# Kernel tuning notes

Hardware: AMD Instinct MI355X
Metric: run time of the kernel (lower is better)

Reference implementation:

```python
import jax, jax.numpy as jnp
import numpy as np

S, B, C, H, M = 384, 8, 1024, 16, 1536
CC = C // H


def setup_inputs() -> dict:
    key = jax.random.key(0)
    ks = jax.random.split(key, 8)
    x = jax.random.normal(ks[0], (S, B, C), dtype=jnp.float32)
    pe = jax.random.normal(ks[1], (S, B, C), dtype=jnp.float32)
    memory_k = jax.random.normal(ks[2], (M, B, H, CC), dtype=jnp.float32)
    memory_v = jax.random.normal(ks[3], (M, B, H, CC), dtype=jnp.float32)
    w_qkv = jax.random.normal(ks[4], (C, 3 * C), dtype=jnp.float32) * 0.02
    b_qkv = jnp.zeros((3 * C,), dtype=jnp.float32)
    w_out = jax.random.normal(ks[5], (C, C), dtype=jnp.float32) * 0.02
    b_out = jnp.zeros((C,), dtype=jnp.float32)
    terminal = jnp.zeros((B,), dtype=bool)
    # causal mask over the new tokens: True = masked (future positions)
    content_mask = jnp.broadcast_to(
        (jnp.arange(S)[None, :] > jnp.arange(S)[:, None])[:, :, None], (S, S, B))
    padding_mask = jnp.zeros((S, B), dtype=bool)  # True = padded
    memory_length = jax.random.randint(ks[6], (B,), 0, M, dtype=jnp.int32)
    return dict(x=x, positional_encoding=pe, memory_k=memory_k, memory_v=memory_v,
                w_qkv=w_qkv, b_qkv=b_qkv, w_out=w_out, b_out=b_out,
                terminal=terminal, content_mask=content_mask,
                padding_mask=padding_mask, memory_length=memory_length)


def reference(x, positional_encoding, memory_k, memory_v, w_qkv, b_qkv,
              w_out, b_out, terminal, content_mask, padding_mask, memory_length):
    s, b, c = x.shape
    # qkv projection
    qkv = (x + positional_encoding) @ w_qkv + b_qkv          # [s,b,3c]
    q, k, v = jnp.split(qkv, 3, axis=-1)
    q = q.reshape(s, b, H, CC)
    k = k.reshape(s, b, H, CC)
    v = v.reshape(s, b, H, CC)
    # clear_memory(terminal): zero lengths for terminal episodes
    mem_len = jnp.where(terminal, 0, memory_length)          # [b]
    # ragged memory concat expressed with fixed capacity M + padding mask
    k_full = jnp.concatenate([memory_k, k], axis=0)          # [M+s,b,H,CC]
    v_full = jnp.concatenate([memory_v, v], axis=0)
    mem_pad = jnp.arange(M)[:, None] >= mem_len[None, :]     # [M,b] True=masked
    kv_pad = jnp.concatenate([mem_pad, padding_mask], axis=0)  # [M+s,b]
    mem_content = jnp.zeros((s, M, b), dtype=bool)           # memory visible to all queries
    full_content = jnp.concatenate([mem_content, content_mask], axis=1)  # [s,M+s,b]
    mask = full_content | kv_pad[None, :, :]                 # [s,M+s,b]
    # attention
    scores = jnp.einsum('sbhc,tbhc->stbh', q, k_full) * (1.0 / np.sqrt(CC))
    scores = jnp.where(mask[:, :, :, None], jnp.float32(-1e9), scores)
    p = jax.nn.softmax(scores, axis=1)                       # [s,M+s,b,h]
    out = jnp.einsum('stbh,tbhc->sbhc', p, v_full).reshape(s, b, c)
    return out @ w_out + b_out
```

## Files before the change

### kernel.cpp

```cpp
#include <hip/hip_runtime.h>
#include <math.h>

#define S_DIM 384
#define B_DIM 8
#define C_DIM 1024
#define H_DIM 16
#define M_DIM 1536
#define CC_DIM 64
#define ROWS  (S_DIM * B_DIM)
#define N3C   (3 * C_DIM)
#define CHUNK 6
#define MAXS  5

typedef unsigned short u16;
typedef short bf8v  __attribute__((ext_vector_type(8)));
typedef short bf4v  __attribute__((ext_vector_type(4)));
typedef u16   us8   __attribute__((ext_vector_type(8)));
typedef u16   us4   __attribute__((ext_vector_type(4)));
typedef float f4v   __attribute__((ext_vector_type(4)));

__device__ __forceinline__ u16 f2bf(float f) {
    unsigned u = __float_as_uint(f);
    u += 0x7fffu + ((u >> 16) & 1u);
    return (u16)(u >> 16);
}
__device__ __forceinline__ float bf2f(u16 v) {
    return __uint_as_float(((unsigned)v) << 16);
}
#if __has_builtin(__builtin_amdgcn_exp2f)
#define EX2(x) __builtin_amdgcn_exp2f(x)
#else
#define EX2(x) __expf((x) * 0.69314718056f)
#endif
#define QSCALE (0.125f * 1.44269504f)

__device__ __forceinline__ unsigned cvtpk_bf16(float a, float b) {
    unsigned r;
    asm("v_cvt_pk_bf16_f32 %0, %1, %2" : "=v"(r) : "v"(a), "v"(b));
    return r;
}

__device__ __forceinline__ f4v mfma16x16x16bf16(bf4v a, bf4v b, f4v c) {
#if __has_builtin(__builtin_amdgcn_mfma_f32_16x16x16bf16_1k)
    return __builtin_amdgcn_mfma_f32_16x16x16bf16_1k(a, b, c, 0, 0, 0);
#else
    return c;
#endif
}

__device__ __forceinline__ void gload16(const u16* g, u16* l) {
    __builtin_amdgcn_global_load_lds(
        (const __attribute__((address_space(1))) void*)g,
        (__attribute__((address_space(3))) void*)l, 16, 0, 0);
}

__device__ __forceinline__ void tr_direct8(const float* __restrict__ in,
                                           u16* __restrict__ out,
                                           int R, int Cc, int r0, int c0, int tid) {
    const int c4 = c0 + (tid & 15) * 4;
    const int rq = r0 + (tid >> 4) * 8;
    float4 L[8];
    #pragma unroll
    for (int k = 0; k < 8; k++)
        L[k] = *(const float4*)(in + (size_t)(rq + k) * Cc + c4);
    #pragma unroll
    for (int j = 0; j < 4; j++) {
        us8 o;
        #pragma unroll
        for (int k = 0; k < 8; k++)
            o[k] = f2bf(((const float*)&L[k])[j]);
        *(us8*)(out + (size_t)(c4 + j) * R + rq) = o;
    }
}

__global__ __launch_bounds__(256) void prep_all(
    const float* __restrict__ x, const float* __restrict__ pe, u16* __restrict__ Abf,
    const float* __restrict__ wqkv, u16* __restrict__ Wqkvt,
    const float* __restrict__ wout, u16* __restrict__ Woutt,
    const float* __restrict__ mk, u16* __restrict__ mk_bf,
    const float* __restrict__ mv, u16* __restrict__ mv_t,
    const unsigned char* __restrict__ terminal, const int* __restrict__ mem_len)
{
    const int bid = blockIdx.x, tid = threadIdx.x;

    if (bid < 1536) {
        const int bh = bid & 127, tg = bid >> 7;
        const int t0 = tg * 128;
        const int b = bh >> 4;
        const int L = terminal[b] ? 0 : mem_len[b];
        const int Lc = ((L + 63) >> 6) << 6;
        if (t0 >= Lc) return;
        const int cc4 = (tid & 15) * 4;
        const int tq = t0 + (tid >> 4) * 8;
        float4 Lv[8];
        #pragma unroll
        for (int k = 0; k < 8; k++)
            Lv[k] = *(const float4*)(mv + ((size_t)(tq + k) * 128 + bh) * 64 + cc4);
        #pragma unroll
        for (int j = 0; j < 4; j++) {
            us8 o;
            #pragma unroll
            for (int k = 0; k < 8; k++)
                o[k] = f2bf(((const float*)&Lv[k])[j]);
            *(us8*)(mv_t + ((size_t)bh * 64 + cc4 + j) * M_DIM + tq) = o;
        }
    } else if (bid < 4608) {
        const int b6 = bid - 1536;
        const int b = b6 & 7, t0 = (b6 >> 3) * 4;
        const int L = terminal[b] ? 0 : mem_len[b];
        const int Lc = ((L + 63) >> 6) << 6;
        if (t0 >= Lc) return;
        const int r = t0 + (tid >> 6);
        const size_t rb = (size_t)r * 8192 + (size_t)b * 1024;
        const int cw = (tid & 63) * 4;
        float4 v[4];
        #pragma unroll
        for (int j = 0; j < 4; j++)
            v[j] = *(const float4*)(mk + rb + cw + j * 256);
        #pragma unroll
        for (int j = 0; j < 4; j++) {
            us4 o;
            o[0] = f2bf(v[j].x); o[1] = f2bf(v[j].y);
            o[2] = f2bf(v[j].z); o[3] = f2bf(v[j].w);
            *(us4*)(mk_bf + rb + cw + j * 256) = o;
        }
    } else if (bid < 5376) {
        size_t i0 = (size_t)(bid - 4608) * 4096 + tid * 16;
        float4 xv[4], pv[4];
        #pragma unroll
        for (int j = 0; j < 4; j++) {
            xv[j] = *(const float4*)(x + i0 + j * 4);
            pv[j] = *(const float4*)(pe + i0 + j * 4);
        }
        #pragma unroll
        for (int h8 = 0; h8 < 2; h8++) {
            us8 o;
            #pragma unroll
            for (int j = 0; j < 2; j++) {
                float4 a = xv[h8 * 2 + j], p = pv[h8 * 2 + j];
                o[j * 4 + 0] = f2bf(a.x + p.x);
                o[j * 4 + 1] = f2bf(a.y + p.y);
                o[j * 4 + 2] = f2bf(a.z + p.z);
                o[j * 4 + 3] = f2bf(a.w + p.w);
            }
            *(us8*)(Abf + i0 + h8 * 8) = o;
        }
    } else if (bid < 5760) {
        const int b2 = bid - 5376;
        tr_direct8(wqkv, Wqkvt, C_DIM, N3C, (b2 / 48) * 128, (b2 % 48) * 64, tid);
    } else {
        const int b3 = bid - 5760;
        tr_direct8(wout, Woutt, C_DIM, C_DIM, (b3 / 16) * 128, (b3 % 16) * 64, tid);
    }
}

__global__ __launch_bounds__(256) void qkv_gemm(
    const u16* __restrict__ Abf, const u16* __restrict__ Wt,
    const float* __restrict__ bias,
    u16* __restrict__ Qw, u16* __restrict__ Kw, u16* __restrict__ Vwt)
{
    __shared__ u16 smem[128 * 64 + 64 * 64];
    u16* As = smem;
    u16* Bs = smem + 128 * 64;
    u16* Cs = smem;

    const int tid = threadIdx.x;
    const int lane = tid & 63, w = tid >> 6;
    const int lr = lane & 15, quad = lane >> 4;
    const int wm = w >> 1, wn = w & 1;
    const int row0 = blockIdx.y * 128, col0 = blockIdx.x * 64;

    f4v acc[4][2];
    #pragma unroll
    for (int i = 0; i < 4; i++)
        #pragma unroll
        for (int j = 0; j < 2; j++)
            acc[i][j] = (f4v){0.f, 0.f, 0.f, 0.f};

    for (int k0 = 0; k0 < C_DIM; k0 += 64) {
        __syncthreads();
        #pragma unroll
        for (int j = 0; j < 4; j++) {
            int idx = j * 256 + tid;
            int r = idx >> 3, c = (idx & 7) ^ (r & 7);
            gload16(&Abf[(size_t)(row0 + r) * C_DIM + k0 + c * 8], &As[idx * 8]);
        }
        #pragma unroll
        for (int j = 0; j < 2; j++) {
            int idx = j * 256 + tid;
            int r = idx >> 3, c = (idx & 7) ^ (r & 7);
            gload16(&Wt[(size_t)(col0 + r) * C_DIM + k0 + c * 8], &Bs[idx * 8]);
        }
        __syncthreads();
        #pragma unroll
        for (int kh = 0; kh < 2; kh++) {
            bf8v a[4], b[2];
            #pragma unroll
            for (int mi = 0; mi < 4; mi++) {
                int row = wm * 64 + mi * 16 + lr;
                int p = (kh * 4 + quad) ^ (lr & 7);
                a[mi] = *(const bf8v*)&As[row * 64 + p * 8];
            }
            #pragma unroll
            for (int nj = 0; nj < 2; nj++) {
                int row = wn * 32 + nj * 16 + lr;
                int p = (kh * 4 + quad) ^ (lr & 7);
                b[nj] = *(const bf8v*)&Bs[row * 64 + p * 8];
            }
            #pragma unroll
            for (int mi = 0; mi < 4; mi++)
                #pragma unroll
                for (int nj = 0; nj < 2; nj++)
                    acc[mi][nj] = __builtin_amdgcn_mfma_f32_16x16x32_bf16(a[mi], b[nj], acc[mi][nj], 0, 0, 0);
        }
    }

    const int which = col0 >> 10;
    const int h = (col0 >> 6) & 15;
    const float qs = (which == 0) ? QSCALE : 1.0f;

    __syncthreads();
    #pragma unroll
    for (int nj = 0; nj < 2; nj++) {
        int col = col0 + wn * 32 + nj * 16 + lr;
        float bv = bias[col];
        #pragma unroll
        for (int mi = 0; mi < 4; mi++)
            #pragma unroll
            for (int reg = 0; reg < 4; reg++)
                Cs[(wm * 64 + mi * 16 + quad * 4 + reg) * 72 + wn * 32 + nj * 16 + lr] =
                    f2bf((acc[mi][nj][reg] + bv) * qs);
    }
    __syncthreads();

    if (which != 2) {
        u16* dstbuf = (which == 0) ? Qw : Kw;
        int r = tid >> 1, half = tid & 1;
        int rg = row0 + r, s = rg >> 3, bb = rg & 7;
        u16* drow = dstbuf + ((size_t)(bb * 16 + h) * S_DIM + s) * 64 + half * 32;
        #pragma unroll
        for (int i = 0; i < 4; i++)
            *(us8*)(drow + i * 8) = *(const us8*)&Cs[r * 72 + half * 32 + i * 8];
    } else {
        int cc = tid & 63, w4 = tid >> 6;
        int s0 = row0 >> 3;
        #pragma unroll
        for (int pb = 0; pb < 2; pb++) {
            int bb = w4 * 2 + pb;
            us8 v0, v1;
            #pragma unroll
            for (int sl = 0; sl < 8; sl++) {
                v0[sl] = Cs[(sl * 8 + bb) * 72 + cc];
                v1[sl] = Cs[((sl + 8) * 8 + bb) * 72 + cc];
            }
            u16* dr = Vwt + ((size_t)(bb * 16 + h) * 64 + cc) * S_DIM + s0;
            *(us8*)dr = v0;
            *(us8*)(dr + 8) = v1;
        }
    }
}

__global__ __launch_bounds__(256) void attn_split(
    const u16* __restrict__ Qw, const u16* __restrict__ Kw,
    const u16* __restrict__ mk_bf, const u16* __restrict__ Vwt,
    const u16* __restrict__ mv_t, const unsigned char* __restrict__ terminal,
    const int* __restrict__ mem_len, u16* __restrict__ Op, float* __restrict__ ml)
{
    __shared__ u16 KsAll[4][64 * 64];
    __shared__ u16 VsAll[4][64 * 64];

    const int tid = threadIdx.x;
    const int lane = tid & 63, w = tid >> 6;
    const int lr = lane & 15, quad = lane >> 4, q8 = quad * 8;
    const int bid = blockIdx.x;
    const int j = bid % MAXS;
    const int g = bid / MAXS;
    const int b = g & 7, h = (g >> 3) & 15, sc = g >> 7;
    const int bh = b * 16 + h, sq0 = sc * 64;
    const int L = terminal[b] ? 0 : mem_len[b];
    const int memChunks = (L + 63) >> 6;
    const int total = memChunks + sc + 1;
    const int lo = j * CHUNK;
    const int hi = (lo + CHUNK < total) ? lo + CHUNK : total;
    if (lo >= total) return;

    const int qrow = sq0 + w * 16 + lr;

    const u16* qbase = Qw + ((size_t)bh * S_DIM + sq0 + w * 16 + lr) * 64;
    bf8v qf0 = *(const bf8v*)&qbase[q8];
    bf8v qf1 = *(const bf8v*)&qbase[32 + q8];

    f4v O[4];
    #pragma unroll
    for (int nj = 0; nj < 4; nj++) O[nj] = (f4v){0.f, 0.f, 0.f, 0.f};
    float m_i = -1e30f, l_i = 0.0f;

    const f4v zero = (f4v){0.f, 0.f, 0.f, 0.f};

    auto stagef = [&](int ch, int buf) {
        const bool isMem = (ch < memChunks);
        const int tloc = isMem ? ch * 64 : (ch - memChunks) * 64;
        const u16* kb; unsigned kstr;
        if (isMem) { kb = mk_bf + ((size_t)tloc * 128 + bh) * 64; kstr = 128u * 64u; }
        else       { kb = Kw + ((size_t)bh * S_DIM + tloc) * 64; kstr = 64u; }
        const u16* vb; unsigned vstr;
        if (isMem) { vb = mv_t + (size_t)bh * 64 * M_DIM + tloc; vstr = M_DIM; }
        else       { vb = Vwt + (size_t)bh * 64 * S_DIM + tloc; vstr = S_DIM; }
        u16* KsB = &KsAll[buf][0];
        u16* VsB = &VsAll[buf][0];
        #pragma unroll
        for (int jj = 0; jj < 2; jj++) {
            int idx = jj * 256 + tid;
            unsigned r = idx >> 3, c = (idx & 7) ^ (r & 7);
            gload16(kb + r * kstr + c * 8u, &KsB[idx * 8]);
        }
        #pragma unroll
        for (int jj = 0; jj < 2; jj++) {
            int idx = jj * 256 + tid;
            unsigned cc = idx >> 3, c = (idx & 7) ^ (cc & 7);
            gload16(vb + cc * vstr + c * 8u, &VsB[idx * 8]);
        }
    };

    stagef(lo, 0);
    if (lo + 1 < hi) stagef(lo + 1, 1);

    for (int ch = lo; ch < hi; ch++) {
        if (ch + 2 < hi) {
            stagef(ch + 2, (ch + 2 - lo) & 3);
            asm volatile("s_waitcnt vmcnt(8)" ::: "memory");
        } else if (ch + 1 < hi) {
            asm volatile("s_waitcnt vmcnt(4)" ::: "memory");
        } else {
            asm volatile("s_waitcnt vmcnt(0)" ::: "memory");
        }
        __builtin_amdgcn_sched_barrier(0);
        __builtin_amdgcn_s_barrier();
        __builtin_amdgcn_sched_barrier(0);

        const u16* Ks = &KsAll[(ch - lo) & 3][0];
        const u16* Vs = &VsAll[(ch - lo) & 3][0];
        const bool isMem = (ch < memChunks);
        const int tloc = isMem ? ch * 64 : (ch - memChunks) * 64;

        f4v sv[4];
        __builtin_amdgcn_s_setprio(1);
        #pragma unroll
        for (int tt = 0; tt < 4; tt++) {
            int row = tt * 16 + lr;
            int p0 = quad ^ (lr & 7), p1 = (4 + quad) ^ (lr & 7);
            bf8v k0 = *(const bf8v*)&Ks[row * 64 + p0 * 8];
            bf8v k1 = *(const bf8v*)&Ks[row * 64 + p1 * 8];
            sv[tt] = __builtin_amdgcn_mfma_f32_16x16x32_bf16(k0, qf0, zero, 0, 0, 0);
            sv[tt] = __builtin_amdgcn_mfma_f32_16x16x32_bf16(k1, qf1, sv[tt], 0, 0, 0);
        }
        __builtin_amdgcn_s_setprio(0);

        if (isMem) {
            if (tloc + 64 > L) {
                #pragma unroll
                for (int tt = 0; tt < 4; tt++)
                    #pragma unroll
                    for (int reg = 0; reg < 4; reg++) {
                        int t = tloc + tt * 16 + quad * 4 + reg;
                        if (t >= L) sv[tt][reg] = -1e30f;
                    }
            }
        } else {
            if (tloc + 63 > sq0 + w * 16) {
                #pragma unroll
                for (int tt = 0; tt < 4; tt++)
                    #pragma unroll
                    for (int reg = 0; reg < 4; reg++) {
                        int t = tloc + tt * 16 + quad * 4 + reg;
                        if (t > qrow) sv[tt][reg] = -1e30f;
                    }
            }
        }

        float rowmax = fmaxf(fmaxf(sv[0][0], sv[0][1]), fmaxf(sv[0][2], sv[0][3]));
        #pragma unroll
        for (int tt = 1; tt < 4; tt++)
            rowmax = fmaxf(rowmax, fmaxf(fmaxf(sv[tt][0], sv[tt][1]),
                                         fmaxf(sv[tt][2], sv[tt][3])));
        rowmax = fmaxf(rowmax, __shfl_xor(rowmax, 16));
        rowmax = fmaxf(rowmax, __shfl_xor(rowmax, 32));

        const bool defer = __all(rowmax - m_i <= 8.0f);
        const float mnew = defer ? m_i : fmaxf(m_i, rowmax);

        float p[16];
        float s0 = 0.f, s1 = 0.f, s2 = 0.f, s3 = 0.f;
        #pragma unroll
        for (int tt = 0; tt < 4; tt++) {
            p[tt * 4 + 0] = EX2(sv[tt][0] - mnew);
            p[tt * 4 + 1] = EX2(sv[tt][1] - mnew);
            p[tt * 4 + 2] = EX2(sv[tt][2] - mnew);
            p[tt * 4 + 3] = EX2(sv[tt][3] - mnew);
            s0 += p[tt * 4 + 0]; s1 += p[tt * 4 + 1];
            s2 += p[tt * 4 + 2]; s3 += p[tt * 4 + 3];
        }
        float sum = (s0 + s1) + (s2 + s3);
        sum += __shfl_xor(sum, 16);
        sum += __shfl_xor(sum, 32);

        bf4v pf[4];
        #pragma unroll
        for (int tt = 0; tt < 4; tt++) {
            union { bf4v v; unsigned u[2]; } pu;
            pu.u[0] = cvtpk_bf16(p[tt * 4 + 0], p[tt * 4 + 1]);
            pu.u[1] = cvtpk_bf16(p[tt * 4 + 2], p[tt * 4 + 3]);
            pf[tt] = pu.v;
        }

        if (defer) {
            l_i += sum;
        } else {
            float alpha = EX2(m_i - mnew);
            m_i = mnew;
            l_i = l_i * alpha + sum;
            float alphaR[4];
            #pragma unroll
            for (int reg = 0; reg < 4; reg++)
                alphaR[reg] = __shfl(alpha, quad * 4 + reg);
            #pragma unroll
            for (int nj = 0; nj < 4; nj++)
                #pragma unroll
                for (int reg = 0; reg < 4; reg++)
                    O[nj][reg] *= alphaR[reg];
        }

        __builtin_amdgcn_s_setprio(1);
        #pragma unroll
        for (int tt = 0; tt < 4; tt++) {
            #pragma unroll
            for (int nj = 0; nj < 4; nj++) {
                int cc = nj * 16 + lr;
                int c = (tt * 2 + (quad >> 1)) ^ (lr & 7);
                bf4v vf = *(const bf4v*)&Vs[cc * 64 + c * 8 + (quad & 1) * 4];
                O[nj] = mfma16x16x16bf16(pf[tt], vf, O[nj]);
            }
        }
        __builtin_amdgcn_s_setprio(0);
    }

    const size_t pbase = (size_t)(g * MAXS + j) * 64;
    if (quad == 0) {
        int row = w * 16 + lr;
        float2 mlv = {m_i, l_i};
        *(float2*)&ml[(pbase + row) * 2] = mlv;
    }
    #pragma unroll
    for (int reg = 0; reg < 4; reg++) {
        int row = w * 16 + quad * 4 + reg;
        #pragma unroll
        for (int nj = 0; nj < 4; nj++)
            Op[(pbase + row) * 64 + nj * 16 + lr] = f2bf(O[nj][reg]);
    }
}

__global__ __launch_bounds__(256) void attn_combine(
    const unsigned char* __restrict__ terminal, const int* __restrict__ mem_len,
    const u16* __restrict__ Op, const float* __restrict__ ml, u16* __restrict__ Obf)
{
    const int g = blockIdx.x;
    const int b = g & 7, h = (g >> 3) & 15, sc = g >> 7;
    const int tid = threadIdx.x;
    const int row = tid >> 2, c0 = (tid & 3) * 16;

    const int L = terminal[b] ? 0 : mem_len[b];
    const int total = ((L + 63) >> 6) + sc + 1;
    const int nsp = (total + CHUNK - 1) / CHUNK;

    float m[MAXS], lv[MAXS];
    #pragma unroll
    for (int j = 0; j < MAXS; j++) {
        if (j < nsp) {
            size_t base = (size_t)(g * MAXS + j) * 64 + row;
            m[j]  = ml[base * 2];
            lv[j] = ml[base * 2 + 1];
        } else { m[j] = -1e30f; lv[j] = 0.0f; }
    }
    float mstar = m[0];
    #pragma unroll
    for (int j = 1; j < MAXS; j++) mstar = fmaxf(mstar, m[j]);
    float sc_j[MAXS], l = 0.0f;
    #pragma unroll
    for (int j = 0; j < MAXS; j++) {
        sc_j[j] = (j < nsp) ? EX2(m[j] - mstar) : 0.0f;
        l += sc_j[j] * lv[j];
    }
    float inv = 1.0f / l;

    float o[16];
    #pragma unroll
    for (int c = 0; c < 16; c++) o[c] = 0.0f;
    for (int j = 0; j < nsp; j++) {
        const u16* src = &Op[((size_t)(g * MAXS + j) * 64 + row) * 64 + c0];
        us8 v0 = *(const us8*)src;
        us8 v1 = *(const us8*)(src + 8);
        #pragma unroll
        for (int c = 0; c < 8; c++) {
            o[c]     += sc_j[j] * bf2f(v0[c]);
            o[c + 8] += sc_j[j] * bf2f(v1[c]);
        }
    }
    int s = sc * 64 + row;
    size_t dst = ((size_t)s * 8 + b) * C_DIM + h * 64 + c0;
    us8 w0, w1;
    #pragma unroll
    for (int c = 0; c < 8; c++) {
        w0[c] = f2bf(o[c] * inv);
        w1[c] = f2bf(o[c + 8] * inv);
    }
    *(us8*)&Obf[dst] = w0;
    *(us8*)&Obf[dst + 8] = w1;
}

__global__ __launch_bounds__(256) void proj_gemm(
    const u16* __restrict__ Abf, const u16* __restrict__ Wt,
    const float* __restrict__ bias, float* __restrict__ out)
{
    __shared__ u16 As[64 * 64];
    __shared__ u16 Bs[64 * 64];
    const int tid = threadIdx.x;
    const int lane = tid & 63, w = tid >> 6;
    const int lr = lane & 15, quad = lane >> 4;
    const int row0 = blockIdx.y * 64, col0 = blockIdx.x * 64;

    f4v acc[4];
    #pragma unroll
    for (int i = 0; i < 4; i++) acc[i] = (f4v){0.f, 0.f, 0.f, 0.f};

    for (int k0 = 0; k0 < C_DIM; k0 += 64) {
        __syncthreads();
        #pragma unroll
        for (int j = 0; j < 2; j++) {
            int idx = j * 256 + tid;
            int r = idx >> 3, c = (idx & 7) ^ (r & 7);
            gload16(&Abf[(size_t)(row0 + r) * C_DIM + k0 + c * 8], &As[idx * 8]);
            gload16(&Wt[(size_t)(col0 + r) * C_DIM + k0 + c * 8], &Bs[idx * 8]);
        }
        __syncthreads();
        #pragma unroll
        for (int kh = 0; kh < 2; kh++) {
            int p = (kh * 4 + quad) ^ (lr & 7);
            bf8v a = *(const bf8v*)&As[(w * 16 + lr) * 64 + p * 8];
            #pragma unroll
            for (int nj = 0; nj < 4; nj++) {
                bf8v bfr = *(const bf8v*)&Bs[(nj * 16 + lr) * 64 + p * 8];
                acc[nj] = __builtin_amdgcn_mfma_f32_16x16x32_bf16(a, bfr, acc[nj], 0, 0, 0);
            }
        }
    }

    #pragma unroll
    for (int nj = 0; nj < 4; nj++) {
        int col = col0 + nj * 16 + lr;
        float bv = bias[col];
        #pragma unroll
        for (int reg = 0; reg < 4; reg++) {
            int rg = row0 + w * 16 + quad * 4 + reg;
            out[(size_t)rg * C_DIM + col] = acc[nj][reg] + bv;
        }
    }
}

extern "C" void kernel_launch(void* const* d_in, const int* in_sizes, int n_in,
                              void* d_out, int out_size, void* d_ws, size_t ws_size,
                              hipStream_t stream) {
    const float* x    = (const float*)d_in[0];
    const float* pe   = (const float*)d_in[1];
    const float* mk   = (const float*)d_in[2];
    const float* mv   = (const float*)d_in[3];
    const float* wqkv = (const float*)d_in[4];
    const float* bqkv = (const float*)d_in[5];
    const float* wout = (const float*)d_in[6];
    const float* bout = (const float*)d_in[7];
    const unsigned char* term = (const unsigned char*)d_in[8];
    const int* mem_len = (const int*)d_in[11];

    char* ws = (char*)d_ws;
    u16* Abf   = (u16*)(ws + 0);
    u16* Obf   = (u16*)(ws + 0);
    u16* Wqkvt = (u16*)(ws + 6291456);
    float* ml  = (float*)(ws + 6291456);
    u16* Woutt = (u16*)(ws + 12582912);
    u16* mk_bf = (u16*)(ws + 14680064);
    u16* mv_t  = (u16*)(ws + 39845888);
    u16* Qw    = (u16*)(ws + 65011712);
    u16* Kw    = (u16*)(ws + 71303168);
    u16* Vwt   = (u16*)(ws + 77594624);
    u16* Op    = (u16*)(ws + 83886080);

    float* out = (float*)d_out;

    prep_all<<<5888, 256, 0, stream>>>(x, pe, Abf, wqkv, Wqkvt, wout, Woutt,
                                       mk, mk_bf, mv, mv_t, term, mem_len);

    qkv_gemm<<<dim3(N3C / 64, ROWS / 128), 256, 0, stream>>>(
        Abf, Wqkvt, bqkv, Qw, Kw, Vwt);

    attn_split<<<B_DIM * H_DIM * (S_DIM / 64) * MAXS, 256, 0, stream>>>(
        Qw, Kw, mk_bf, Vwt, mv_t, term, mem_len, Op, ml);

    attn_combine<<<B_DIM * H_DIM * (S_DIM / 64), 256, 0, stream>>>(
        term, mem_len, Op, ml, Obf);

    proj_gemm<<<dim3(C_DIM / 64, ROWS / 64), 256, 0, stream>>>(
        Obf, Woutt, bout, out);
}
```

Baseline: 289.6 us.

## Load K/V fragments directly from global memory instead of staged LDS pipeline

Removes the four-buffer LDS staging of K and V tiles, along with its async global-to-LDS loads, vmcnt waits and block barriers. Each wave now reads its MFMA operands for K and V straight from global memory (through the caches). This drops the LDS footprint and barrier synchronisation, but the four waves now each fetch the same K/V data redundantly and the load latency is no longer hidden by the prefetch pipeline.

New measurement: 413.6 us. 1.43x slower.

```diff
diff --git a/kernel.cpp b/kernel.cpp
--- a/kernel.cpp
+++ b/kernel.cpp
@@ -266,9 +266,6 @@
     const u16* __restrict__ mv_t, const unsigned char* __restrict__ terminal,
     const int* __restrict__ mem_len, u16* __restrict__ Op, float* __restrict__ ml)
 {
-    __shared__ u16 KsAll[4][64 * 64];
-    __shared__ u16 VsAll[4][64 * 64];
-
     const int tid = threadIdx.x;
     const int lane = tid & 63, w = tid >> 6;
     const int lr = lane & 15, quad = lane >> 4, q8 = quad * 8;
@@ -297,7 +294,7 @@
 
     const f4v zero = (f4v){0.f, 0.f, 0.f, 0.f};
 
-    auto stagef = [&](int ch, int buf) {
+    for (int ch = lo; ch < hi; ch++) {
         const bool isMem = (ch < memChunks);
         const int tloc = isMem ? ch * 64 : (ch - memChunks) * 64;
         const u16* kb; unsigned kstr;
@@ -306,51 +303,14 @@
         const u16* vb; unsigned vstr;
         if (isMem) { vb = mv_t + (size_t)bh * 64 * M_DIM + tloc; vstr = M_DIM; }
         else       { vb = Vwt + (size_t)bh * 64 * S_DIM + tloc; vstr = S_DIM; }
-        u16* KsB = &KsAll[buf][0];
-        u16* VsB = &VsAll[buf][0];
-        #pragma unroll
-        for (int jj = 0; jj < 2; jj++) {
-            int idx = jj * 256 + tid;
-            unsigned r = idx >> 3, c = (idx & 7) ^ (r & 7);
-            gload16(kb + r * kstr + c * 8u, &KsB[idx * 8]);
-        }
-        #pragma unroll
-        for (int jj = 0; jj < 2; jj++) {
-            int idx = jj * 256 + tid;
-            unsigned cc = idx >> 3, c = (idx & 7) ^ (cc & 7);
-            gload16(vb + cc * vstr + c * 8u, &VsB[idx * 8]);
-        }
-    };
-
-    stagef(lo, 0);
-    if (lo + 1 < hi) stagef(lo + 1, 1);
-
-    for (int ch = lo; ch < hi; ch++) {
-        if (ch + 2 < hi) {
-            stagef(ch + 2, (ch + 2 - lo) & 3);
-            asm volatile("s_waitcnt vmcnt(8)" ::: "memory");
-        } else if (ch + 1 < hi) {
-            asm volatile("s_waitcnt vmcnt(4)" ::: "memory");
-        } else {
-            asm volatile("s_waitcnt vmcnt(0)" ::: "memory");
-        }
-        __builtin_amdgcn_sched_barrier(0);
-        __builtin_amdgcn_s_barrier();
-        __builtin_amdgcn_sched_barrier(0);
-
-        const u16* Ks = &KsAll[(ch - lo) & 3][0];
-        const u16* Vs = &VsAll[(ch - lo) & 3][0];
-        const bool isMem = (ch < memChunks);
-        const int tloc = isMem ? ch * 64 : (ch - memChunks) * 64;
 
         f4v sv[4];
         __builtin_amdgcn_s_setprio(1);
         #pragma unroll
         for (int tt = 0; tt < 4; tt++) {
-            int row = tt * 16 + lr;
-            int p0 = quad ^ (lr & 7), p1 = (4 + quad) ^ (lr & 7);
-            bf8v k0 = *(const bf8v*)&Ks[row * 64 + p0 * 8];
-            bf8v k1 = *(const bf8v*)&Ks[row * 64 + p1 * 8];
+            unsigned row = tt * 16 + lr;
+            bf8v k0 = *(const bf8v*)(kb + row * kstr + q8);
+            bf8v k1 = *(const bf8v*)(kb + row * kstr + 32 + q8);
             sv[tt] = __builtin_amdgcn_mfma_f32_16x16x32_bf16(k0, qf0, zero, 0, 0, 0);
             sv[tt] = __builtin_amdgcn_mfma_f32_16x16x32_bf16(k1, qf1, sv[tt], 0, 0, 0);
         }
@@ -435,9 +395,8 @@
         for (int tt = 0; tt < 4; tt++) {
             #pragma unroll
             for (int nj = 0; nj < 4; nj++) {
-                int cc = nj * 16 + lr;
-                int c = (tt * 2 + (quad >> 1)) ^ (lr & 7);
-                bf4v vf = *(const bf4v*)&Vs[cc * 64 + c * 8 + (quad & 1) * 4];
+                unsigned cc = nj * 16 + lr;
+                bf4v vf = *(const bf4v*)(vb + cc * vstr + tt * 16 + quad * 4);
                 O[nj] = mfma16x16x16bf16(pf[tt], vf, O[nj]);
             }
         }
```
